# Optimization experiments

Hardware: AMD Instinct MI355X
Metric: run time of the kernel (lower is better)

## Reference

```python
import jax, jax.numpy as jnp
import numpy as np

B, H, W = 64, 256, 256
G = 64
V = G * G          # 4096
HID = 512
S = 50


def _conv(x, w, b):
    # x: (B,C,H,W), w: (O,I,3,3) -> 'same' conv, NCHW
    y = jax.lax.conv_general_dilated(x, w, (1, 1), 'SAME',
                                     dimension_numbers=('NCHW', 'OIHW', 'NCHW'))
    return y + b[None, :, None, None]


def setup_inputs() -> dict:
    key = jax.random.key(0)
    ks = jax.random.split(key, 14)

    def lin(k, shape, fan_in):
        return (jax.random.normal(k, shape, jnp.float32) / np.float32(np.sqrt(fan_in)))

    return {
        'mask': jax.random.uniform(ks[0], (B, 1, H, W), jnp.float32),
        'target_ids': jax.random.randint(ks[1], (B, S), 0, V),
        'conv1_w': lin(ks[2], (16, 1, 3, 3), 9), 'conv1_b': jnp.zeros((16,), jnp.float32),
        'conv2_w': lin(ks[3], (32, 16, 3, 3), 16 * 9), 'conv2_b': jnp.zeros((32,), jnp.float32),
        'feat_w': lin(ks[4], (HID, 32), 32), 'feat_b': jnp.zeros((HID,), jnp.float32),
        'ctx_w': lin(ks[5], (HID, HID), HID), 'ctx_b': jnp.zeros((HID,), jnp.float32),
        'tok_emb': jax.random.normal(ks[6], (V + 1, HID), jnp.float32) * 0.02,
        'w_ih': lin(ks[7], (4 * HID, HID), HID), 'w_hh': lin(ks[8], (4 * HID, HID), HID),
        'b_ih': jnp.zeros((4 * HID,), jnp.float32), 'b_hh': jnp.zeros((4 * HID,), jnp.float32),
        'head_w': lin(ks[9], (V, HID), HID), 'head_b': jnp.zeros((V,), jnp.float32),
    }


def reference(mask, target_ids, conv1_w, conv1_b, conv2_w, conv2_b,
              feat_w, feat_b, ctx_w, ctx_b, tok_emb,
              w_ih, w_hh, b_ih, b_hh, head_w, head_b):
    b = mask.shape[0]
    vocab = head_w.shape[0]

    # --- CNN encoder ---
    x = jax.nn.relu(_conv(mask, conv1_w, conv1_b))                    # (B,16,H,W)
    x = jax.lax.reduce_window(x, -jnp.inf, jax.lax.max,
                              (1, 1, 2, 2), (1, 1, 2, 2), 'VALID')    # (B,16,H/2,W/2)
    x = jax.nn.relu(_conv(x, conv2_w, conv2_b))                       # (B,32,H/2,W/2)
    x = x.mean(axis=(2, 3))                                           # AdaptiveAvgPool2d(1) -> (B,32)

    h0 = x @ feat_w.T + feat_b                                        # (B,HID)
    c0 = jnp.zeros_like(h0)
    ctx = h0 @ ctx_w.T + ctx_b                                        # (B,HID)

    # Full teacher forcing (ratio=1.0): input token at t=0 is start token V,
    # at t>0 it is target_ids[:, t-1]. All embeddings gathered upfront.
    start = jnp.full((b, 1), vocab, dtype=target_ids.dtype)
    toks = jnp.concatenate([start, target_ids[:, :-1]], axis=1)       # (B,S)
    embs = tok_emb[toks]                                              # (B,S,HID)
    lstm_in = jnp.swapaxes(embs, 0, 1) + ctx[None]                    # (S,B,HID)

    bias = b_ih + b_hh

    def step(carry, inp):
        h, c = carry
        gates = inp @ w_ih.T + h @ w_hh.T + bias                      # (B,4*HID)
        i, f, g, o = jnp.split(gates, 4, axis=-1)
        c = jax.nn.sigmoid(f) * c + jax.nn.sigmoid(i) * jnp.tanh(g)
        h = jax.nn.sigmoid(o) * jnp.tanh(c)
        logit = h @ head_w.T + head_b                                 # (B,V)
        return (h, c), logit

    _, logits = jax.lax.scan(step, (h0, c0), lstm_in)                 # (S,B,V)
    return jnp.swapaxes(logits, 0, 1)                                 # (B,S,V)
```

## Files before the change

### kernel.cpp

```cpp
#include <hip/hip_runtime.h>
#include <cmath>

typedef __attribute__((ext_vector_type(8))) _Float16 f16x8;
typedef __attribute__((ext_vector_type(2))) _Float16 f16x2;
typedef __attribute__((ext_vector_type(4))) float f32x4;
typedef __attribute__((ext_vector_type(4))) unsigned u32x4;

#define LSTM_NB 32
#define CONV_NB 2048
#define PREP_NB 1536

__device__ __forceinline__ unsigned short f2h(float x) {
  return __builtin_bit_cast(unsigned short, (_Float16)x);
}

__device__ __forceinline__ void h2f2(unsigned u, float& a, float& b) {
  a = (float)__builtin_bit_cast(_Float16, (unsigned short)(u & 0xffffu));
  b = (float)__builtin_bit_cast(_Float16, (unsigned short)(u >> 16));
}

__device__ __forceinline__ float dot2(unsigned a, unsigned b, float c) {
#if __has_builtin(__builtin_amdgcn_fdot2)
  return __builtin_amdgcn_fdot2(__builtin_bit_cast(f16x2, a),
                                __builtin_bit_cast(f16x2, b), c, false);
#else
  f16x2 av = __builtin_bit_cast(f16x2, a), bv = __builtin_bit_cast(f16x2, b);
  return fmaf((float)av[0], (float)bv[0], fmaf((float)av[1], (float)bv[1], c));
#endif
}

__device__ __forceinline__ void gload16(const void* g, void* l) {
  __builtin_amdgcn_global_load_lds(
      (const __attribute__((address_space(1))) void*)g,
      (__attribute__((address_space(3))) void*)l, 16, 0, 0);
}

__device__ __forceinline__ void cload16(const void* p, u32x4* dst) {
  asm volatile("global_load_dwordx4 %0, %1, off sc0 sc1"
               : "=v"(*dst)
               : "v"(p));
}

__global__ __launch_bounds__(512) void k_conv(
    const float* __restrict__ mask, const float* __restrict__ w1,
    const float* __restrict__ b1, const float* __restrict__ w2,
    const float* __restrict__ b2, float* __restrict__ part,
    const float* __restrict__ wih, const float* __restrict__ hw,
    unsigned short* __restrict__ wihb, unsigned short* __restrict__ hwb,
    int* __restrict__ flags)
{
  __shared__ unsigned short s_mask[38 * 72];
  __shared__ unsigned s_p1p[8][18 * 36];
  __shared__ unsigned s_w2p[32][8][9];
  __shared__ float s_w1[144];
  __shared__ float s_b1[16];
  __shared__ float s_b2[32];

  const int tid = threadIdx.x;

  if (blockIdx.x >= CONV_NB) {
    const int i = (blockIdx.x - CONV_NB) * 512 + tid;
    if (i < 6400) flags[i] = 0;
    if (i < 262144) {
      float4 v = *(const float4*)(wih + (size_t)i * 4);
      unsigned lo = (unsigned)f2h(v.x) | ((unsigned)f2h(v.y) << 16);
      unsigned hi = (unsigned)f2h(v.z) | ((unsigned)f2h(v.w) << 16);
      *(uint2*)(wihb + (size_t)i * 4) = make_uint2(lo, hi);
    } else {
      const int j = i - 262144;
      float4 v = *(const float4*)(hw + (size_t)j * 4);
      unsigned lo = (unsigned)f2h(v.x) | ((unsigned)f2h(v.y) << 16);
      unsigned hi = (unsigned)f2h(v.z) | ((unsigned)f2h(v.w) << 16);
      *(uint2*)(hwb + (size_t)j * 4) = make_uint2(lo, hi);
    }
    return;
  }

  const int b = blockIdx.x >> 5;
  const int tile = blockIdx.x & 31;
  const int px0 = (tile & 3) * 32, py0 = (tile >> 2) * 16;
  const float* mb = mask + (size_t)b * 65536;
  const int gr0 = 2 * py0 - 3, gc0 = 2 * px0 - 3;

  for (int i = tid; i < 144; i += 512) s_w1[i] = w1[i];
  for (int i = tid; i < 2304; i += 512) {
    int oc = i / 72, p8 = (i % 72) / 9, k = i % 9;
    unsigned lo = f2h(w2[(size_t)(oc * 16 + 2 * p8) * 9 + k]);
    unsigned hi = f2h(w2[(size_t)(oc * 16 + 2 * p8 + 1) * 9 + k]);
    s_w2p[oc][p8][k] = lo | (hi << 16);
  }
  if (tid < 16) s_b1[tid] = b1[tid];
  if (tid < 32) s_b2[tid] = b2[tid];

  for (int idx = tid; idx < 38 * 70; idx += 512) {
    int r = idx / 70, cc = idx - r * 70;
    int gr = gr0 + r, gc = gc0 + cc;
    float v = (gr >= 0 && gr < 256 && gc >= 0 && gc < 256)
                  ? mb[gr * 256 + gc] : 0.f;
    s_mask[r * 72 + cc] = f2h(v);
  }
  __syncthreads();

  for (int idx = tid; idx < 18 * 34; idx += 512) {
    int ly = idx / 34, lx = idx - ly * 34;
    int py = py0 - 1 + ly, px = px0 - 1 + lx;
    if (py < 0 || py >= 128 || px < 0 || px >= 128) {
      for (int p8 = 0; p8 < 8; p8++) s_p1p[p8][ly * 36 + lx] = 0;
    } else {
      float patch[4][4];
      const unsigned short* pm = &s_mask[(2 * ly) * 72 + 2 * lx];
#pragma unroll
      for (int i = 0; i < 4; i++) {
        unsigned d0 = *(const unsigned*)(pm + i * 72);
        unsigned d1 = *(const unsigned*)(pm + i * 72 + 2);
        h2f2(d0, patch[i][0], patch[i][1]);
        h2f2(d1, patch[i][2], patch[i][3]);
      }
      float m[16];
      for (int o = 0; o < 16; o++) {
        float mm = 0.f;
#pragma unroll
        for (int dy = 0; dy < 2; dy++)
#pragma unroll
          for (int dx = 0; dx < 2; dx++) {
            float v = s_b1[o];
#pragma unroll
            for (int ky = 0; ky < 3; ky++)
#pragma unroll
              for (int kx = 0; kx < 3; kx++)
                v = fmaf(patch[dy + ky][dx + kx], s_w1[o * 9 + ky * 3 + kx], v);
            mm = fmaxf(mm, v);
          }
        m[o] = mm;
      }
#pragma unroll
      for (int p8 = 0; p8 < 8; p8++)
        s_p1p[p8][ly * 36 + lx] =
            (unsigned)f2h(m[2 * p8]) | ((unsigned)f2h(m[2 * p8 + 1]) << 16);
    }
  }
  __syncthreads();

  const int ocg = tid >> 6;
  const int sp = tid & 63;
  const int sx = (sp & 7) * 4, sy = (sp >> 3) * 2;
  float acc[4][8];
#pragma unroll
  for (int a = 0; a < 4; a++)
#pragma unroll
    for (int q = 0; q < 8; q++) acc[a][q] = 0.f;

  for (int p8 = 0; p8 < 8; p8++) {
    unsigned pp[4][6];
#pragma unroll
    for (int i = 0; i < 4; i++) {
      const unsigned* row = &s_p1p[p8][(sy + i) * 36 + sx];
      u32x4 q4 = *(const u32x4*)row;
      uint2 q2 = *(const uint2*)(row + 4);
      pp[i][0] = q4[0]; pp[i][1] = q4[1]; pp[i][2] = q4[2]; pp[i][3] = q4[3];
      pp[i][4] = q2.x;  pp[i][5] = q2.y;
    }
#pragma unroll
    for (int o4 = 0; o4 < 4; o4++) {
      const unsigned* w = &s_w2p[ocg * 4 + o4][p8][0];
      unsigned w00 = w[0], w01 = w[1], w02 = w[2];
      unsigned w10 = w[3], w11 = w[4], w12 = w[5];
      unsigned w20 = w[6], w21 = w[7], w22 = w[8];
#pragma unroll
      for (int y = 0; y < 2; y++)
#pragma unroll
        for (int x = 0; x < 4; x++) {
          float s = acc[o4][y * 4 + x];
          s = dot2(pp[y][x], w00, s);
          s = dot2(pp[y][x + 1], w01, s);
          s = dot2(pp[y][x + 2], w02, s);
          s = dot2(pp[y + 1][x], w10, s);
          s = dot2(pp[y + 1][x + 1], w11, s);
          s = dot2(pp[y + 1][x + 2], w12, s);
          s = dot2(pp[y + 2][x], w20, s);
          s = dot2(pp[y + 2][x + 1], w21, s);
          s = dot2(pp[y + 2][x + 2], w22, s);
          acc[o4][y * 4 + x] = s;
        }
    }
  }

  const int lane = tid & 63;
#pragma unroll
  for (int o4 = 0; o4 < 4; o4++) {
    float bv = s_b2[ocg * 4 + o4];
    float s = 0.f;
#pragma unroll
    for (int q = 0; q < 8; q++) s += fmaxf(acc[o4][q] + bv, 0.f);
    for (int off = 32; off > 0; off >>= 1) s += __shfl_down(s, off, 64);
    if (lane == 0) part[(b * 32 + tile) * 32 + ocg * 4 + o4] = s;
  }
}

__global__ __launch_bounds__(256) void k_pool_ctx(
    const float* __restrict__ part, const float* __restrict__ feat_w,
    const float* __restrict__ feat_b, const float* __restrict__ ctx_w,
    const float* __restrict__ ctx_b, float* __restrict__ h0,
    unsigned short* __restrict__ h0f, float* __restrict__ ctx)
{
  const int b = blockIdx.x, tid = threadIdx.x;
  __shared__ float pl[32];
  __shared__ float hs[512];
  if (tid < 32) {
    float s = 0.f;
    for (int t = 0; t < 32; t++) s += part[(b * 32 + t) * 32 + tid];
    pl[tid] = s * (1.0f / 16384.0f);
  }
  __syncthreads();
  for (int j = tid; j < 512; j += 256) {
    float acc = feat_b[j];
    const float* w = feat_w + j * 32;
#pragma unroll
    for (int ic = 0; ic < 32; ic++) acc = fmaf(pl[ic], w[ic], acc);
    h0[b * 512 + j] = acc;
    h0f[b * 512 + j] = f2h(acc);
    hs[j] = acc;
  }
  __syncthreads();
  for (int j = tid; j < 512; j += 256) {
    const float* w = ctx_w + (size_t)j * 512;
    float s0 = 0.f, s1 = 0.f, s2 = 0.f, s3 = 0.f;
    for (int k = 0; k < 512; k += 4) {
      float4 w4 = *(const float4*)(w + k);
      s0 = fmaf(hs[k], w4.x, s0);
      s1 = fmaf(hs[k + 1], w4.y, s1);
      s2 = fmaf(hs[k + 2], w4.z, s2);
      s3 = fmaf(hs[k + 3], w4.w, s3);
    }
    ctx[b * 512 + j] = ctx_b[j] + ((s0 + s1) + (s2 + s3));
  }
}

__global__ __launch_bounds__(256) void k_zero_f(float* __restrict__ p) {
  p[blockIdx.x * 256 + threadIdx.x] = 0.f;
}

template <int MODE>
__global__ __launch_bounds__(256) void k_gemm_mfma(
    const unsigned short* __restrict__ A, const unsigned short* __restrict__ B,
    const float* __restrict__ bias_a, const float* __restrict__ bias_b,
    float* __restrict__ C, int NB, const int* __restrict__ tgt,
    const float* __restrict__ temb, const float* __restrict__ ctx)
{
  __shared__ unsigned short sA[128 * 32];
  __shared__ unsigned short sB[128 * 32];
  const int tid = threadIdx.x;
  const int bx = blockIdx.x % NB, by = blockIdx.x / NB;
  const int lane = tid & 63, wv = tid >> 6;
  const int wr = wv >> 1, wc = wv & 1;
  const unsigned short* Bb = B + (size_t)bx * 128 * 512;

  f32x4 acc[4][4];
#pragma unroll
  for (int m = 0; m < 4; m++)
#pragma unroll
    for (int n = 0; n < 4; n++) acc[m][n] = (f32x4){0.f, 0.f, 0.f, 0.f};

  const int r0 = tid >> 2, c0 = (tid & 3) * 8;
  const int idx1 = tid + 256;
  const int r1 = idx1 >> 2, c1 = (idx1 & 3) * 8;
  unsigned short* lA0 = sA + (size_t)wv * 512;
  unsigned short* lA1 = sA + 2048 + (size_t)wv * 512;
  unsigned short* lB0 = sB + (size_t)wv * 512;
  unsigned short* lB1 = sB + 2048 + (size_t)wv * 512;

  size_t arow0 = 0, arow1 = 0;
  const float *e0 = nullptr, *e1 = nullptr, *cp0 = nullptr, *cp1 = nullptr;
  if (MODE == 0) {
    const int lr0 = by * 128 + r0;
    const int lr1 = lr0 + 64;
    const int t0 = lr0 >> 6, b0 = lr0 & 63;
    const int t1 = lr1 >> 6, b1 = lr1 & 63;
    const int tok0 = (t0 == 0) ? 4096 : tgt[b0 * 50 + (t0 - 1)];
    const int tok1 = (t1 == 0) ? 4096 : tgt[b1 * 50 + (t1 - 1)];
    e0 = temb + (size_t)tok0 * 512;
    e1 = temb + (size_t)tok1 * 512;
    cp0 = ctx + b0 * 512;
    cp1 = ctx + b1 * 512;
  } else {
    const int lr0 = by * 128 + r0, lr1 = by * 128 + r1;
    arow0 = (size_t)((lr0 % 50) * 64 + lr0 / 50) * 512;
    arow1 = (size_t)((lr1 % 50) * 64 + lr1 / 50) * 512;
  }

  const int frow = lane & 15;
  const int foff = (lane >> 4) * 8;

  for (int kc = 0; kc < 512; kc += 32) {
    if (MODE == 0) {
      float4 ea = *(const float4*)(e0 + kc + c0);
      float4 eb = *(const float4*)(e0 + kc + c0 + 4);
      float4 ca = *(const float4*)(cp0 + kc + c0);
      float4 cb = *(const float4*)(cp0 + kc + c0 + 4);
      u32x4 p0;
      p0[0] = (unsigned)f2h(ea.x + ca.x) | ((unsigned)f2h(ea.y + ca.y) << 16);
      p0[1] = (unsigned)f2h(ea.z + ca.z) | ((unsigned)f2h(ea.w + ca.w) << 16);
      p0[2] = (unsigned)f2h(eb.x + cb.x) | ((unsigned)f2h(eb.y + cb.y) << 16);
      p0[3] = (unsigned)f2h(eb.z + cb.z) | ((unsigned)f2h(eb.w + cb.w) << 16);
      *(u32x4*)(sA + tid * 8) = p0;
      float4 ea1 = *(const float4*)(e1 + kc + c1);
      float4 eb1 = *(const float4*)(e1 + kc + c1 + 4);
      float4 ca1 = *(const float4*)(cp1 + kc + c1);
      float4 cb1 = *(const float4*)(cp1 + kc + c1 + 4);
      u32x4 p1;
      p1[0] = (unsigned)f2h(ea1.x + ca1.x) | ((unsigned)f2h(ea1.y + ca1.y) << 16);
      p1[1] = (unsigned)f2h(ea1.z + ca1.z) | ((unsigned)f2h(ea1.w + ca1.w) << 16);
      p1[2] = (unsigned)f2h(eb1.x + cb1.x) | ((unsigned)f2h(eb1.y + cb1.y) << 16);
      p1[3] = (unsigned)f2h(eb1.z + cb1.z) | ((unsigned)f2h(eb1.w + cb1.w) << 16);
      *(u32x4*)(sA + 2048 + tid * 8) = p1;
    } else {
      gload16(A + arow0 + kc + c0, lA0);
      gload16(A + arow1 + kc + c1, lA1);
    }
    gload16(Bb + (size_t)r0 * 512 + kc + c0, lB0);
    gload16(Bb + (size_t)r1 * 512 + kc + c1, lB1);
    __syncthreads();

    f16x8 af[4], bfr[4];
#pragma unroll
    for (int m = 0; m < 4; m++)
      af[m] = *(const f16x8*)(sA + (wr * 64 + m * 16 + frow) * 32 + foff);
#pragma unroll
    for (int n = 0; n < 4; n++)
      bfr[n] = *(const f16x8*)(sB + (wc * 64 + n * 16 + frow) * 32 + foff);
#pragma unroll
    for (int m = 0; m < 4; m++)
#pragma unroll
      for (int n = 0; n < 4; n++)
        acc[m][n] = __builtin_amdgcn_mfma_f32_16x16x32_f16(
            af[m], bfr[n], acc[m][n], 0, 0, 0);
    __syncthreads();
  }

#pragma unroll
  for (int n = 0; n < 4; n++) {
    const int gc = bx * 128 + wc * 64 + n * 16 + (lane & 15);
    const float bv = (MODE == 0) ? (bias_a[gc] + bias_b[gc]) : bias_a[gc];
#pragma unroll
    for (int m = 0; m < 4; m++) {
      const int rb = by * 128 + wr * 64 + m * 16 + (lane >> 4) * 4;
#pragma unroll
      for (int j = 0; j < 4; j++) {
        const int r = rb + j;
        float v = acc[m][n][j] + bv;
        if (MODE == 0) {
          int t = r >> 6, bb = r & 63;
          C[(size_t)t * 131072 + (size_t)gc * 64 + bb] = v;
        } else {
          C[(size_t)r * 4096 + gc] = v;
        }
      }
    }
  }
}

__global__ __launch_bounds__(256, 1) void k_lstm_mfma(
    const float* __restrict__ xgT,
    const float* __restrict__ w_hh,
    const unsigned short* __restrict__ h0f,
    unsigned short* __restrict__ hallf,
    int* __restrict__ flags)
{
  __shared__ unsigned short s_h[64 * 512];
  __shared__ float s_g[4][64][17];
  const int tid = threadIdx.x;
  const int kb = blockIdx.x;
  const int g = tid >> 6;
  const int lane = tid & 63;
  const int frow = lane & 15;
  const int foff = (lane >> 4) * 8;

  f16x8 wf[16];
  {
    const float* wrow = w_hh + (size_t)(g * 512 + kb * 16 + frow) * 512;
#pragma unroll
    for (int kf = 0; kf < 16; kf++) {
      float tmp[8];
      *(float4*)tmp = *(const float4*)(wrow + kf * 32 + foff);
      *(float4*)(tmp + 4) = *(const float4*)(wrow + kf * 32 + foff + 4);
#pragma unroll
      for (int j = 0; j < 8; j++) wf[kf][j] = (_Float16)tmp[j];
    }
  }

  float c[4] = {0.f, 0.f, 0.f, 0.f};
  const int b2 = tid & 63, dd2 = tid >> 6;

  for (int t = 0; t < 50; ++t) {
    const unsigned short* H = t ? hallf + (size_t)(t - 1) * 32768 : h0f;

    const float* xr =
        xgT + (size_t)t * 131072 + (size_t)(kb * 16 + dd2 * 4) * 64 + b2;
    float xv[16];
#pragma unroll
    for (int gq = 0; gq < 4; gq++)
#pragma unroll
      for (int i = 0; i < 4; i++)
        xv[gq * 4 + i] = xr[(size_t)(gq * 512 + i) * 64];

    if (t > 0 && tid < 32) {
      while (__hip_atomic_load(&flags[(t - 1) * 32 + tid], __ATOMIC_RELAXED,
                               __HIP_MEMORY_SCOPE_AGENT) == 0) {
        __builtin_amdgcn_s_sleep(1);
      }
    }
    __syncthreads();

    {
      u32x4 r[16];
#pragma unroll
      for (int i = 0; i < 16; i++)
        cload16((const char*)H + (size_t)(tid + i * 256) * 16, &r[i]);
      asm volatile("s_waitcnt vmcnt(0)" ::: "memory");
      __builtin_amdgcn_sched_barrier(0);
#pragma unroll
      for (int i = 0; i < 16; i++) {
        int byte = (tid + i * 256) * 16;
        int swz = byte ^ (((byte >> 10) & 7) << 4);
        *(u32x4*)((char*)s_h + swz) = r[i];
      }
    }
    __syncthreads();

    f32x4 acc[4];
#pragma unroll
    for (int mt = 0; mt < 4; mt++) acc[mt] = (f32x4){0.f, 0.f, 0.f, 0.f};
#pragma unroll
    for (int kf = 0; kf < 16; kf++) {
#pragma unroll
      for (int mt = 0; mt < 4; mt++) {
        const int row = mt * 16 + frow;
        const int byte = (row << 10) + kf * 64 + foff * 2;
        const int swz = byte ^ ((row & 7) << 4);
        f16x8 ah = *(const f16x8*)((const char*)s_h + swz);
        acc[mt] =
            __builtin_amdgcn_mfma_f32_16x16x32_f16(ah, wf[kf], acc[mt], 0, 0, 0);
      }
    }
#pragma unroll
    for (int mt = 0; mt < 4; mt++)
#pragma unroll
      for (int j = 0; j < 4; j++)
        s_g[g][mt * 16 + (lane >> 4) * 4 + j][frow] = acc[mt][j];
    __syncthreads();

    unsigned long long qf = 0;
#pragma unroll
    for (int i = 0; i < 4; i++) {
      float gi = s_g[0][b2][dd2 * 4 + i] + xv[0 + i];
      float gf = s_g[1][b2][dd2 * 4 + i] + xv[4 + i];
      float gg = s_g[2][b2][dd2 * 4 + i] + xv[8 + i];
      float go = s_g[3][b2][dd2 * 4 + i] + xv[12 + i];
      float ig = 1.f / (1.f + expf(-gi));
      float fg = 1.f / (1.f + expf(-gf));
      float og = 1.f / (1.f + expf(-go));
      float gt = tanhf(gg);
      c[i] = fmaf(fg, c[i], ig * gt);
      float h = og * tanhf(c[i]);
      qf |= (unsigned long long)f2h(h) << (16 * i);
    }
    const size_t ho = (size_t)b2 * 512 + kb * 16 + dd2 * 4;
    __hip_atomic_store((unsigned long long*)(hallf + (size_t)t * 32768 + ho),
                       qf, __ATOMIC_RELAXED, __HIP_MEMORY_SCOPE_AGENT);
    __syncthreads();
    if (t < 49 && tid == 0)
      __hip_atomic_store(&flags[t * 32 + kb], 1, __ATOMIC_RELAXED,
                         __HIP_MEMORY_SCOPE_AGENT);
  }
}

__global__ __launch_bounds__(256) void k_lstm_step1(
    const float* __restrict__ xgT, const float* __restrict__ w_hh,
    const float* __restrict__ hin, float* __restrict__ hout,
    unsigned short* __restrict__ hallf_t, float* __restrict__ cbuf, int t)
{
  __shared__ float s_w[8][512];
  __shared__ float s_g[2][4][64];
  const int tid = threadIdx.x;
  const int dd0 = blockIdx.x * 2;

  for (int idx = tid; idx < 1024; idx += 256) {
    int row = idx >> 7;
    int k4 = (idx & 127) << 2;
    int q_ = row >> 1, dd_i = row & 1;
    *(float4*)&s_w[row][k4] =
        *(const float4*)(w_hh + (size_t)(q_ * 512 + dd0 + dd_i) * 512 + k4);
  }
  const int b = tid & 63;
  const int q = tid >> 6;
  __syncthreads();

  const float* hc = hin + b * 512;
  const float* xr = xgT + (size_t)t * 131072 + (size_t)(q * 512 + dd0) * 64 + b;
  float a0 = xr[0], a1 = xr[64];
  const float* w0 = s_w[q * 2 + 0];
  const float* w1 = s_w[q * 2 + 1];
#pragma unroll 8
  for (int k = 0; k < 512; k += 4) {
    float4 h4 = *(const float4*)(hc + k);
    float4 u = *(const float4*)(w0 + k);
    float4 v = *(const float4*)(w1 + k);
    a0 = fmaf(h4.x, u.x, fmaf(h4.y, u.y, fmaf(h4.z, u.z, fmaf(h4.w, u.w, a0))));
    a1 = fmaf(h4.x, v.x, fmaf(h4.y, v.y, fmaf(h4.z, v.z, fmaf(h4.w, v.w, a1))));
  }
  s_g[0][q][b] = a0;
  s_g[1][q][b] = a1;
  __syncthreads();
  if (q < 2) {
    const int dd = dd0 + q;
    float gi = s_g[q][0][b], gf = s_g[q][1][b];
    float gg = s_g[q][2][b], go = s_g[q][3][b];
    float ig = 1.f / (1.f + expf(-gi));
    float fg = 1.f / (1.f + expf(-gf));
    float og = 1.f / (1.f + expf(-go));
    float gt = tanhf(gg);
    float c = fmaf(fg, cbuf[b * 512 + dd], ig * gt);
    float h = og * tanhf(c);
    cbuf[b * 512 + dd] = c;
    hout[b * 512 + dd] = h;
    hallf_t[(size_t)b * 512 + dd] = f2h(h);
  }
}

extern "C" void kernel_launch(void* const* d_in, const int* in_sizes, int n_in,
                              void* d_out, int out_size, void* d_ws,
                              size_t ws_size, hipStream_t stream) {
  const float* mask   = (const float*)d_in[0];
  const int*   tgt    = (const int*)d_in[1];
  const float* w1     = (const float*)d_in[2];
  const float* b1     = (const float*)d_in[3];
  const float* w2     = (const float*)d_in[4];
  const float* b2     = (const float*)d_in[5];
  const float* feat_w = (const float*)d_in[6];
  const float* feat_b = (const float*)d_in[7];
  const float* ctx_w  = (const float*)d_in[8];
  const float* ctx_b  = (const float*)d_in[9];
  const float* temb   = (const float*)d_in[10];
  const float* w_ih   = (const float*)d_in[11];
  const float* w_hh_p = (const float*)d_in[12];
  const float* b_ih   = (const float*)d_in[13];
  const float* b_hh   = (const float*)d_in[14];
  const float* head_w = (const float*)d_in[15];
  const float* head_b = (const float*)d_in[16];

  float* ws = (float*)d_ws;
  float* part  = ws;
  float* hbuf  = ws + 65536;
  float* ctx   = ws + 131072;
  int*   flags = (int*)(ws + 163840);
  unsigned short* h0f  = (unsigned short*)(ws + 170240);
  unsigned short* hallf = (unsigned short*)(ws + 186624);
  unsigned short* wihb = (unsigned short*)(ws + 1005824);
  unsigned short* hwb  = (unsigned short*)(ws + 1530112);
  float* xgT   = ws + 2578688;
  float* cbuf  = part;
  float* out   = (float*)d_out;

  k_conv<<<CONV_NB + PREP_NB, 512, 0, stream>>>(
      mask, w1, b1, w2, b2, part, w_ih, head_w, wihb, hwb, flags);
  k_pool_ctx<<<64, 256, 0, stream>>>(part, feat_w, feat_b, ctx_w, ctx_b,
                                     hbuf, h0f, ctx);
  k_gemm_mfma<0><<<25 * 16, 256, 0, stream>>>(
      nullptr, wihb, b_ih, b_hh, xgT, 16, tgt, temb, ctx);

  {
    const float* xgT_c = xgT;
    const float* whh_c = w_hh_p;
    const unsigned short* h0f_c = h0f;
    unsigned short* hallf_c = hallf;
    int* flags_c = flags;
    void* args[] = {(void*)&xgT_c, (void*)&whh_c, (void*)&h0f_c,
                    (void*)&hallf_c, (void*)&flags_c};
    hipError_t e = hipLaunchCooperativeKernel(
        (const void*)k_lstm_mfma, dim3(LSTM_NB), dim3(256), args, 0, stream);
    if (e != hipSuccess) {
      (void)hipGetLastError();
      k_zero_f<<<128, 256, 0, stream>>>(cbuf);
      for (int t = 0; t < 50; t++) {
        const float* hin = hbuf + (t & 1) * 32768;
        float* hout = hbuf + ((t + 1) & 1) * 32768;
        k_lstm_step1<<<256, 256, 0, stream>>>(
            xgT, w_hh_p, hin, hout, hallf + (size_t)t * 32768, cbuf, t);
      }
    }
  }

  k_gemm_mfma<1><<<25 * 32, 256, 0, stream>>>(
      hallf, hwb, head_b, nullptr, out, 32, nullptr, nullptr, nullptr);
}
```

Before: 522.7 us.

## Replace per-step LSTM flag barrier with NaN-sentinel polling on hidden state

Removes the per-block flag array and its spin-wait and publish barriers between LSTM timesteps. Instead, the hidden-state buffer is prefilled with a half-precision NaN sentinel, and each block polls its loads of the previous step's hidden state, re-reading only the chunks that still contain the sentinel. This drops two __syncthreads and one flag round-trip per step and lets data arrival itself serve as the signal. The cost is sentinel initialization of the whole hidden buffer in the prep kernel. A computed h that happens to equal the sentinel bit pattern, or a torn 8-byte store, could cause wrong results or spinning until the guard limit.

```diff
diff --git a/kernel.cpp b/kernel.cpp
--- a/kernel.cpp
+++ b/kernel.cpp
@@ -9,6 +9,7 @@
 #define LSTM_NB 32
 #define CONV_NB 2048
 #define PREP_NB 1536
+#define SENT64 0x7e007e007e007e00ull
 
 __device__ __forceinline__ unsigned short f2h(float x) {
   return __builtin_bit_cast(unsigned short, (_Float16)x);
@@ -47,7 +48,7 @@
     const float* __restrict__ b2, float* __restrict__ part,
     const float* __restrict__ wih, const float* __restrict__ hw,
     unsigned short* __restrict__ wihb, unsigned short* __restrict__ hwb,
-    int* __restrict__ flags)
+    unsigned long long* __restrict__ hall64)
 {
   __shared__ unsigned short s_mask[38 * 72];
   __shared__ unsigned s_p1p[8][18 * 36];
@@ -60,7 +61,7 @@
 
   if (blockIdx.x >= CONV_NB) {
     const int i = (blockIdx.x - CONV_NB) * 512 + tid;
-    if (i < 6400) flags[i] = 0;
+    if (i < 409600) hall64[i] = SENT64;
     if (i < 262144) {
       float4 v = *(const float4*)(wih + (size_t)i * 4);
       unsigned lo = (unsigned)f2h(v.x) | ((unsigned)f2h(v.y) << 16);
@@ -363,8 +364,7 @@
     const float* __restrict__ xgT,
     const float* __restrict__ w_hh,
     const unsigned short* __restrict__ h0f,
-    unsigned short* __restrict__ hallf,
-    int* __restrict__ flags)
+    unsigned short* __restrict__ hallf)
 {
   __shared__ unsigned short s_h[64 * 512];
   __shared__ float s_g[4][64][17];
@@ -403,21 +403,33 @@
       for (int i = 0; i < 4; i++)
         xv[gq * 4 + i] = xr[(size_t)(gq * 512 + i) * 64];
 
-    if (t > 0 && tid < 32) {
-      while (__hip_atomic_load(&flags[(t - 1) * 32 + tid], __ATOMIC_RELAXED,
-                               __HIP_MEMORY_SCOPE_AGENT) == 0) {
-        __builtin_amdgcn_s_sleep(1);
-      }
-    }
-    __syncthreads();
-
     {
       u32x4 r[16];
-#pragma unroll
-      for (int i = 0; i < 16; i++)
-        cload16((const char*)H + (size_t)(tid + i * 256) * 16, &r[i]);
-      asm volatile("s_waitcnt vmcnt(0)" ::: "memory");
-      __builtin_amdgcn_sched_barrier(0);
+      unsigned stale = 0xffffu;
+      int guard = 0;
+      while (stale) {
+#pragma unroll
+        for (int i = 0; i < 16; i++)
+          if (stale & (1u << i))
+            cload16((const char*)H + (size_t)(tid + i * 256) * 16, &r[i]);
+        asm volatile("s_waitcnt vmcnt(0)" ::: "memory");
+        __builtin_amdgcn_sched_barrier(0);
+        unsigned ns = 0;
+#pragma unroll
+        for (int i = 0; i < 16; i++) {
+          if (stale & (1u << i)) {
+            bool bad = false;
+#pragma unroll
+            for (int j = 0; j < 4; j++) {
+              unsigned w = r[i][j];
+              if ((w & 0xffffu) == 0x7e00u || (w >> 16) == 0x7e00u) bad = true;
+            }
+            if (bad) ns |= (1u << i);
+          }
+        }
+        stale = ns;
+        if (++guard > 100000) break;
+      }
 #pragma unroll
       for (int i = 0; i < 16; i++) {
         int byte = (tid + i * 256) * 16;
@@ -467,10 +479,6 @@
     const size_t ho = (size_t)b2 * 512 + kb * 16 + dd2 * 4;
     __hip_atomic_store((unsigned long long*)(hallf + (size_t)t * 32768 + ho),
                        qf, __ATOMIC_RELAXED, __HIP_MEMORY_SCOPE_AGENT);
-    __syncthreads();
-    if (t < 49 && tid == 0)
-      __hip_atomic_store(&flags[t * 32 + kb], 1, __ATOMIC_RELAXED,
-                         __HIP_MEMORY_SCOPE_AGENT);
   }
 }
 
@@ -552,7 +560,6 @@
   float* part  = ws;
   float* hbuf  = ws + 65536;
   float* ctx   = ws + 131072;
-  int*   flags = (int*)(ws + 163840);
   unsigned short* h0f  = (unsigned short*)(ws + 170240);
   unsigned short* hallf = (unsigned short*)(ws + 186624);
   unsigned short* wihb = (unsigned short*)(ws + 1005824);
@@ -562,7 +569,8 @@
   float* out   = (float*)d_out;
 
   k_conv<<<CONV_NB + PREP_NB, 512, 0, stream>>>(
-      mask, w1, b1, w2, b2, part, w_ih, head_w, wihb, hwb, flags);
+      mask, w1, b1, w2, b2, part, w_ih, head_w, wihb, hwb,
+      (unsigned long long*)hallf);
   k_pool_ctx<<<64, 256, 0, stream>>>(part, feat_w, feat_b, ctx_w, ctx_b,
                                      hbuf, h0f, ctx);
   k_gemm_mfma<0><<<25 * 16, 256, 0, stream>>>(
@@ -573,9 +581,8 @@
     const float* whh_c = w_hh_p;
     const unsigned short* h0f_c = h0f;
     unsigned short* hallf_c = hallf;
-    int* flags_c = flags;
     void* args[] = {(void*)&xgT_c, (void*)&whh_c, (void*)&h0f_c,
-                    (void*)&hallf_c, (void*)&flags_c};
+                    (void*)&hallf_c};
     hipError_t e = hipLaunchCooperativeKernel(
         (const void*)k_lstm_mfma, dim3(LSTM_NB), dim3(256), args, 0, stream);
     if (e != hipSuccess) {
```

Measured after the change: 697.8 us. 33.5% more time.
